# Performance work log

Hardware: AMD Instinct MI355X
Metric: run time of the kernel (lower is better)

## Reference

```python
import jax, jax.numpy as jnp
import numpy as np
import math

V, TB, C, H, L = 50257, 1024, 1024, 16, 8
B, T = 2, 1024
D = C // H


def setup_inputs() -> dict:
    key = jax.random.key(0)
    ks = jax.random.split(key, 16)
    s = 0.02
    n = lambda k, shp: (jax.random.normal(k, shp, jnp.float32) * s)
    inp = {
        "idx": jax.random.randint(ks[0], (B, T), 0, V),
        "tok_emb": n(ks[1], (V, C)),
        "pos_emb": n(ks[2], (1, TB, C)),
        # per-layer stacked params (torch Linear convention: W is [out, in])
        "Wq": n(ks[3], (L, C, C)), "bq": jnp.zeros((L, C)),
        "Wk": n(ks[4], (L, C, C)), "bk": jnp.zeros((L, C)),
        "Wv": n(ks[5], (L, C, C)), "bv": jnp.zeros((L, C)),
        "Wp": n(ks[6], (L, C, C)), "bp": jnp.zeros((L, C)),
        "ln1_w": jnp.ones((L, C)), "ln1_b": jnp.zeros((L, C)),
        "ln2_w": jnp.ones((L, C)), "ln2_b": jnp.zeros((L, C)),
        "W1": n(ks[7], (L, 4 * C, C)), "b1": jnp.zeros((L, 4 * C)),
        "W2": n(ks[8], (L, C, 4 * C)), "b2": jnp.zeros((L, C)),
        "lnf_w": jnp.ones((C,)), "lnf_b": jnp.zeros((C,)),
        "head_w": n(ks[9], (V, C)),
    }
    return inp


def _layer_norm(x, w, b, eps=1e-5):
    mu = x.mean(-1, keepdims=True)
    var = x.var(-1, keepdims=True)
    return (x - mu) * jax.lax.rsqrt(var + eps) * w + b


def _gpt_forward(idx, tok_emb, pos_emb, Wq, bq, Wk, bk, Wv, bv, Wp, bp,
                 ln1_w, ln1_b, ln2_w, ln2_b, W1, b1, W2, b2, lnf_w, lnf_b, head_w):
    b, t = idx.shape
    x = tok_emb[idx] + pos_emb[:, :t, :]  # [B, T, C]; drop = identity (eval)
    causal = jnp.tril(jnp.ones((t, t), dtype=bool))  # [T, T]
    scale = 1.0 / math.sqrt(D)

    def block(x, p):
        (wq, bq_, wk, bk_, wv, bv_, wp, bp_, l1w, l1b, l2w, l2b, w1, b1_, w2, b2_) = p
        h = _layer_norm(x, l1w, l1b)
        q = (h @ wq.T + bq_).reshape(b, t, H, D).transpose(0, 2, 1, 3)  # [B,H,T,D]
        k = (h @ wk.T + bk_).reshape(b, t, H, D).transpose(0, 2, 1, 3)
        v = (h @ wv.T + bv_).reshape(b, t, H, D).transpose(0, 2, 1, 3)
        att = jnp.einsum("bhqd,bhkd->bhqk", q, k) * scale
        att = jnp.where(causal, att, -jnp.inf)
        att = jax.nn.softmax(att, axis=-1)
        y = jnp.einsum("bhqk,bhkd->bhqd", att, v)
        y = y.transpose(0, 2, 1, 3).reshape(b, t, C)
        x = x + (y @ wp.T + bp_)
        h2 = _layer_norm(x, l2w, l2b)
        m = jax.nn.gelu(h2 @ w1.T + b1_, approximate=False)  # torch nn.GELU (erf)
        x = x + (m @ w2.T + b2_)
        return x, None

    params = (Wq, bq, Wk, bk, Wv, bv, Wp, bp, ln1_w, ln1_b, ln2_w, ln2_b, W1, b1, W2, b2)
    x, _ = jax.lax.scan(block, x, params)
    x = _layer_norm(x, lnf_w, lnf_b)
    logits = x @ head_w.T  # [B, T, V]
    return logits


def reference(idx, tok_emb, pos_emb, Wq, bq, Wk, bk, Wv, bv, Wp, bp,
              ln1_w, ln1_b, ln2_w, ln2_b, W1, b1, W2, b2, lnf_w, lnf_b, head_w):
    return _gpt_forward(idx, tok_emb, pos_emb, Wq, bq, Wk, bk, Wv, bv, Wp, bp,
                        ln1_w, ln1_b, ln2_w, ln2_b, W1, b1, W2, b2, lnf_w, lnf_b, head_w)
```

## Files before the change

kernel.cpp:

```cpp
#include <hip/hip_runtime.h>
#include <math.h>

#define V_ 50257
#define C_ 1024
#define H_ 16
#define L_ 8
#define B_ 2
#define T_ 1024
#define BT_ 2048
#define CC_ (C_*C_)
#define QLD_ 3072

typedef unsigned short ushort_t;
using bf16x8 = __attribute__((ext_vector_type(8))) short;
using f32x4  = __attribute__((ext_vector_type(4))) float;

__device__ __forceinline__ ushort_t f2bf(float f){
  union { float f; unsigned u; } a; a.f = f;
  unsigned r = a.u + 0x7fffu + ((a.u >> 16) & 1u);
  return (ushort_t)(r >> 16);
}

__device__ __forceinline__ float wave_sum(float v){
  #pragma unroll
  for(int o=32;o>0;o>>=1) v += __shfl_down(v,o,64);
  return v;
}
__device__ __forceinline__ float wave_max(float v){
  #pragma unroll
  for(int o=32;o>0;o>>=1) v = fmaxf(v, __shfl_down(v,o,64));
  return v;
}

__global__ __launch_bounds__(256) void cvt_blk(const float* __restrict__ s, ushort_t* __restrict__ d,
    long inner4, int nblk, long dstStride4){
  long total = inner4 * nblk;
  for(long i = (long)blockIdx.x*256 + threadIdx.x; i < total; i += (long)gridDim.x*256){
    long blk = i / inner4, r = i - blk*inner4;
    float4 v = ((const float4*)s)[i];
    ushort4 o; o.x=f2bf(v.x); o.y=f2bf(v.y); o.z=f2bf(v.z); o.w=f2bf(v.w);
    ((ushort4*)d)[blk*dstStride4 + r] = o;
  }
}

__global__ __launch_bounds__(256) void pack_qkv_bias(const float* __restrict__ bq,
    const float* __restrict__ bk, const float* __restrict__ bv, float* __restrict__ dst){
  int i = blockIdx.x*256 + threadIdx.x;
  int l = i / QLD_, c = i - l*QLD_;
  float v;
  if(c < C_)            v = bq[l*C_ + c];
  else if(c < 2*C_)     v = bk[l*C_ + c - C_];
  else                  v = bv[l*C_ + c - 2*C_];
  dst[i] = v;
}

__global__ __launch_bounds__(256) void embed_kernel(const int* __restrict__ idx,
    const float* __restrict__ tok, const float* __restrict__ pos, float* __restrict__ x){
  int i = blockIdx.x*256 + threadIdx.x;
  int c = i & (C_-1); int bt = i >> 10; int t = bt & (T_-1);
  x[i] = tok[(size_t)idx[bt]*C_ + c] + pos[t*C_ + c];
}

__global__ __launch_bounds__(256) void ln_kernel(const float* in, const float* __restrict__ w,
    const float* __restrict__ b, float* outF, ushort_t* outB){
  int row = blockIdx.x;
  const float* xr = in + (size_t)row*C_;
  float vals[4]; float sum=0.f, sq=0.f;
  #pragma unroll
  for(int l=0;l<4;l++){ float v = xr[threadIdx.x + l*256]; vals[l]=v; sum+=v; sq+=v*v; }
  __shared__ float r1[4], r2[4];
  float s1 = wave_sum(sum), s2 = wave_sum(sq);
  int wid = threadIdx.x>>6, lane = threadIdx.x&63;
  if(lane==0){ r1[wid]=s1; r2[wid]=s2; }
  __syncthreads();
  float tot  = r1[0]+r1[1]+r1[2]+r1[3];
  float tot2 = r2[0]+r2[1]+r2[2]+r2[3];
  float mu  = tot * (1.f/C_);
  float var = tot2 * (1.f/C_) - mu*mu;
  float inv = rsqrtf(var + 1e-5f);
  #pragma unroll
  for(int l=0;l<4;l++){
    int c = threadIdx.x + l*256;
    float v = (vals[l]-mu)*inv*w[c] + b[c];
    if(outB) outB[(size_t)row*C_ + c] = f2bf(v);
    else     outF[(size_t)row*C_ + c] = v;
  }
}

template<int BN>
__global__ __launch_bounds__(256) void gemm_mfma(
    const ushort_t* __restrict__ A, const ushort_t* __restrict__ W,
    const float* __restrict__ bias, const float* resid,
    float* outF, ushort_t* outB,
    int M, int N, int K, int act)
{
  constexpr int BM = 128;
  constexpr int NSA = BM/16;
  constexpr int NSB = BN/16;
  constexpr int NBF = BN/32;
  __shared__ __align__(16) short sA[2][NSA*512];
  __shared__ __align__(16) short sB[2][NSB*512];
  const int tid  = threadIdx.x;
  const int lane = tid & 63, wid = tid >> 6;
  const int wr = wid >> 1, wc = wid & 1;
  const int m0 = blockIdx.x * BM, n0 = blockIdx.y * BN;
  const int r16 = lane & 15, kq = lane >> 4;

  auto stage = [&](int buf, int k0){
    #pragma unroll
    for(int s2=0; s2<2; ++s2){
      int s = wid*2 + s2;
      const ushort_t* g = A + (size_t)(m0 + s*16 + r16)*K + k0 + kq*8;
      __builtin_amdgcn_global_load_lds((const __attribute__((address_space(1))) void*)g,
          (__attribute__((address_space(3))) void*)&sA[buf][s*512], 16, 0, 0);
    }
    #pragma unroll
    for(int s2=0; s2<NSB/4; ++s2){
      int s = wid*(NSB/4) + s2;
      int gn = n0 + s*16 + r16; if(gn >= N) gn = N-1;
      const ushort_t* g = W + (size_t)gn*K + k0 + kq*8;
      __builtin_amdgcn_global_load_lds((const __attribute__((address_space(1))) void*)g,
          (__attribute__((address_space(3))) void*)&sB[buf][s*512], 16, 0, 0);
    }
  };

  f32x4 acc[4][NBF];
  #pragma unroll
  for(int i=0;i<4;i++)
    #pragma unroll
    for(int j=0;j<NBF;j++) acc[i][j] = (f32x4){0.f,0.f,0.f,0.f};

  const int NT = K >> 5;
  stage(0, 0);
  int cur = 0;
  for(int t=0; t<NT; ++t){
    __syncthreads();
    if(t+1 < NT) stage(cur^1, (t+1)*32);
    bf16x8 af[4], bfr[NBF];
    #pragma unroll
    for(int m=0;m<4;m++) af[m] = *(const bf16x8*)&sA[cur][(wr*4+m)*512 + lane*8];
    #pragma unroll
    for(int n=0;n<NBF;n++) bfr[n] = *(const bf16x8*)&sB[cur][(wc*NBF+n)*512 + lane*8];
    #pragma unroll
    for(int m=0;m<4;m++)
      #pragma unroll
      for(int n=0;n<NBF;n++)
        acc[m][n] = __builtin_amdgcn_mfma_f32_16x16x32_bf16(af[m], bfr[n], acc[m][n], 0, 0, 0);
    cur ^= 1;
  }

  const int colb = n0 + wc*(BN/2);
  #pragma unroll
  for(int m=0;m<4;m++){
    int rowb = m0 + wr*64 + m*16 + kq*4;
    #pragma unroll
    for(int n=0;n<NBF;n++){
      int col = colb + n*16 + r16;
      if(col >= N) continue;
      float bv = bias ? bias[col] : 0.f;
      #pragma unroll
      for(int i=0;i<4;i++){
        int row = rowb + i;
        float v = acc[m][n][i] + bv;
        if(act) v = 0.5f*v*(1.f + erff(v*0.70710678118654752f));
        if(resid) v += resid[(size_t)row*N + col];
        if(outB) outB[(size_t)row*N + col] = f2bf(v);
        else     outF[(size_t)row*N + col] = v;
      }
    }
  }
}

__global__ __launch_bounds__(256) void flash_kernel(const ushort_t* __restrict__ qkv,
    ushort_t* __restrict__ y){
  const int tid = threadIdx.x, lane = tid & 63, wid = tid >> 6;
  const int r16 = lane & 15, kq = lane >> 4;
  const int qt = blockIdx.x, bh = blockIdx.y, b = bh >> 4, h = bh & 15;
  const int q0 = qt*64, qw0 = q0 + wid*16;
  const int qa = qw0 + r16;

  __shared__ __align__(16) short Kt[4][512];
  __shared__ __align__(16) short VT[64][36];
  __shared__ __align__(16) short Pl[4][16][36];
  __shared__ __align__(16) short Ol[4][16][68];

  const size_t rowQ = (size_t)(b*T_ + qw0 + r16)*QLD_ + h*64 + kq*8;
  bf16x8 qf0 = *(const bf16x8*)(qkv + rowQ);
  bf16x8 qf1 = *(const bf16x8*)(qkv + rowQ + 32);

  f32x4 acc[4];
  #pragma unroll
  for(int t=0;t<4;t++) acc[t] = (f32x4){0.f,0.f,0.f,0.f};
  float m_r = -INFINITY, l_r = 0.f;

  const int njt = q0/32 + 2;
  for(int jt=0; jt<njt; ++jt){
    __syncthreads();
    {
      const ushort_t* g = qkv + (size_t)(b*T_ + jt*32 + (wid>>1)*16 + r16)*QLD_
                          + C_ + h*64 + (wid&1)*32 + kq*8;
      __builtin_amdgcn_global_load_lds((const __attribute__((address_space(1))) void*)g,
          (__attribute__((address_space(3))) void*)&Kt[wid][lane*8], 16, 0, 0);
    }
    {
      int k = tid >> 3, d0 = (tid & 7)*8;
      bf16x8 vv = *(const bf16x8*)(qkv + (size_t)(b*T_ + jt*32 + k)*QLD_ + 2*C_ + h*64 + d0);
      #pragma unroll
      for(int j=0;j<8;j++) VT[d0+j][k] = vv[j];
    }
    __syncthreads();

    if(jt*32 <= qw0 + 15){
      f32x4 st0 = (f32x4){0.f,0.f,0.f,0.f}, st1 = st0;
      st0 = __builtin_amdgcn_mfma_f32_16x16x32_bf16(*(const bf16x8*)&Kt[0][lane*8], qf0, st0, 0,0,0);
      st0 = __builtin_amdgcn_mfma_f32_16x16x32_bf16(*(const bf16x8*)&Kt[1][lane*8], qf1, st0, 0,0,0);
      st1 = __builtin_amdgcn_mfma_f32_16x16x32_bf16(*(const bf16x8*)&Kt[2][lane*8], qf0, st1, 0,0,0);
      st1 = __builtin_amdgcn_mfma_f32_16x16x32_bf16(*(const bf16x8*)&Kt[3][lane*8], qf1, st1, 0,0,0);

      float vals[8]; float mx = m_r;
      #pragma unroll
      for(int s=0;s<2;s++){
        #pragma unroll
        for(int i=0;i<4;i++){
          int ka = jt*32 + 16*s + 4*kq + i;
          float v = (s? st1[i] : st0[i]) * 0.125f;
          v = (ka <= qa) ? v : -INFINITY;
          vals[s*4+i] = v; mx = fmaxf(mx, v);
        }
      }
      mx = fmaxf(mx, __shfl_xor(mx, 16, 64));
      mx = fmaxf(mx, __shfl_xor(mx, 32, 64));
      float alpha = __expf(m_r - mx);
      float ps = 0.f;
      #pragma unroll
      for(int idx=0; idx<8; idx++){
        float p = __expf(vals[idx] - mx);
        ps += p;
        Pl[wid][r16][(idx>>2)*16 + 4*kq + (idx&3)] = (short)f2bf(p);
      }
      ps += __shfl_xor(ps, 16, 64);
      ps += __shfl_xor(ps, 32, 64);
      l_r = l_r*alpha + ps; m_r = mx;
      #pragma unroll
      for(int t=0;t<4;t++)
        #pragma unroll
        for(int j=0;j<4;j++) acc[t][j] *= alpha;

      union { bf16x8 v8; uint2 u2[2]; } pf, vf;
      pf.u2[0] = *(const uint2*)&Pl[wid][r16][kq*8];
      pf.u2[1] = *(const uint2*)&Pl[wid][r16][kq*8 + 4];
      #pragma unroll
      for(int db=0; db<4; db++){
        vf.u2[0] = *(const uint2*)&VT[16*db + r16][kq*8];
        vf.u2[1] = *(const uint2*)&VT[16*db + r16][kq*8 + 4];
        acc[db] = __builtin_amdgcn_mfma_f32_16x16x32_bf16(vf.v8, pf.v8, acc[db], 0,0,0);
      }
    }
  }

  float linv = 1.f / l_r;
  #pragma unroll
  for(int db=0; db<4; db++)
    #pragma unroll
    for(int i=0;i<4;i++)
      Ol[wid][r16][16*db + 4*kq + i] = (short)f2bf(acc[db][i]*linv);
  int q = lane >> 2, c0 = (lane & 3)*16;
  const short* src = &Ol[wid][q][c0];
  uint2 a0 = *(const uint2*)(src+0), a1 = *(const uint2*)(src+4);
  uint2 a2 = *(const uint2*)(src+8), a3 = *(const uint2*)(src+12);
  ushort_t* dst = y + (size_t)(b*T_ + qw0 + q)*C_ + h*64 + c0;
  uint4 w0 = {a0.x, a0.y, a1.x, a1.y}, w1 = {a2.x, a2.y, a3.x, a3.y};
  *(uint4*)(dst+0) = w0;
  *(uint4*)(dst+8) = w1;
}

__global__ __launch_bounds__(256) void gemm_nt(const float* __restrict__ A, const float* __restrict__ W,
    const float* __restrict__ bias, const float* resid, float* Cm,
    int M, int N, int K, int act){
  __shared__ float As[16][68];
  __shared__ float Bs[16][68];
  int m0 = blockIdx.y*64, n0 = blockIdx.x*64;
  int tid = threadIdx.x;
  int tx = tid & 15, ty = tid >> 4;
  float acc[4][4] = {};
  for(int k0=0;k0<K;k0+=16){
    #pragma unroll
    for(int l=0;l<4;l++){
      int li = tid + l*256;
      int r = li >> 4, c = li & 15;
      int gm = m0 + r, gn = n0 + r, gk = k0 + c;
      As[c][r] = (gm<M) ? A[(size_t)gm*K + gk] : 0.f;
      Bs[c][r] = (gn<N) ? W[(size_t)gn*K + gk] : 0.f;
    }
    __syncthreads();
    #pragma unroll
    for(int k=0;k<16;k++){
      float4 av = *(const float4*)&As[k][ty*4];
      float4 bv = *(const float4*)&Bs[k][tx*4];
      float a[4] = {av.x, av.y, av.z, av.w};
      float b4[4] = {bv.x, bv.y, bv.z, bv.w};
      #pragma unroll
      for(int i=0;i<4;i++)
        #pragma unroll
        for(int j=0;j<4;j++)
          acc[i][j] = fmaf(a[i], b4[j], acc[i][j]);
    }
    __syncthreads();
  }
  #pragma unroll
  for(int i=0;i<4;i++){
    int m = m0 + ty*4 + i; if(m>=M) continue;
    #pragma unroll
    for(int j=0;j<4;j++){
      int n = n0 + tx*4 + j; if(n>=N) continue;
      float v = acc[i][j];
      if(bias) v += bias[n];
      if(act)  v = 0.5f*v*(1.f + erff(v*0.70710678118654752f));
      if(resid) v += resid[(size_t)m*N + n];
      Cm[(size_t)m*N + n] = v;
    }
  }
}

extern "C" void kernel_launch(void* const* d_in, const int* in_sizes, int n_in,
                              void* d_out, int out_size, void* d_ws, size_t ws_size,
                              hipStream_t stream) {
  const int*   idx  = (const int*)  d_in[0];
  const float* tok  = (const float*)d_in[1];
  const float* pos  = (const float*)d_in[2];
  const float* Wq   = (const float*)d_in[3];
  const float* bq   = (const float*)d_in[4];
  const float* Wk   = (const float*)d_in[5];
  const float* bk   = (const float*)d_in[6];
  const float* Wv   = (const float*)d_in[7];
  const float* bv   = (const float*)d_in[8];
  const float* Wp   = (const float*)d_in[9];
  const float* bp   = (const float*)d_in[10];
  const float* ln1w = (const float*)d_in[11];
  const float* ln1b = (const float*)d_in[12];
  const float* ln2w = (const float*)d_in[13];
  const float* ln2b = (const float*)d_in[14];
  const float* W1   = (const float*)d_in[15];
  const float* b1   = (const float*)d_in[16];
  const float* W2   = (const float*)d_in[17];
  const float* b2   = (const float*)d_in[18];
  const float* lnfw = (const float*)d_in[19];
  const float* lnfb = (const float*)d_in[20];
  const float* headw= (const float*)d_in[21];

  float* out = (float*)d_out;
  ushort_t* qkvb = (ushort_t*)(out);
  ushort_t* hb   = (ushort_t*)(out + 3145728);
  ushort_t* yb   = (ushort_t*)(out + 4194304);
  ushort_t* mb   = (ushort_t*)(out + 5242880);
  ushort_t* wqkv = (ushort_t*)(out + 9437184);
  ushort_t* wpb  = (ushort_t*)(out + 22020096);
  ushort_t* w1b  = (ushort_t*)(out + 26214400);
  ushort_t* w2b  = (ushort_t*)(out + 42991616);
  float*    bqkv = out + 59768832;
  float*    x    = (float*)d_ws;
  ushort_t* xb   = (ushort_t*)((float*)d_ws + 2097152);
  ushort_t* whb  = (ushort_t*)((float*)d_ws + 3145728);
  const bool big = ws_size >= (size_t)28877312 * 4;

  cvt_blk<<<2048,256,0,stream>>>(Wq, wqkv,          CC_/4, L_, 3*CC_/4);
  cvt_blk<<<2048,256,0,stream>>>(Wk, wqkv + CC_,    CC_/4, L_, 3*CC_/4);
  cvt_blk<<<2048,256,0,stream>>>(Wv, wqkv + 2*CC_,  CC_/4, L_, 3*CC_/4);
  cvt_blk<<<2048,256,0,stream>>>(Wp, wpb,  (long)L_*CC_/4,   1, (long)L_*CC_/4);
  cvt_blk<<<2048,256,0,stream>>>(W1, w1b,  (long)L_*CC_,     1, (long)L_*CC_);
  cvt_blk<<<2048,256,0,stream>>>(W2, w2b,  (long)L_*CC_,     1, (long)L_*CC_);
  if(big) cvt_blk<<<2048,256,0,stream>>>(headw, whb, (long)V_*C_/4, 1, (long)V_*C_/4);
  pack_qkv_bias<<<L_*QLD_/256,256,0,stream>>>(bq, bk, bv, bqkv);

  embed_kernel<<<BT_*C_/256, 256, 0, stream>>>(idx, tok, pos, x);

  for(int l=0;l<L_;l++){
    ln_kernel<<<BT_,256,0,stream>>>(x, ln1w + l*C_, ln1b + l*C_, nullptr, hb);
    gemm_mfma<128><<<dim3(BT_/128, QLD_/128),256,0,stream>>>(hb, wqkv + (size_t)l*3*CC_,
        bqkv + l*QLD_, nullptr, nullptr, qkvb, BT_, QLD_, C_, 0);
    flash_kernel<<<dim3(T_/64, B_*H_),256,0,stream>>>(qkvb, yb);
    gemm_mfma<64><<<dim3(BT_/128, C_/64),256,0,stream>>>(yb, wpb + (size_t)l*CC_,
        bp + l*C_, x, x, nullptr, BT_, C_, C_, 0);
    ln_kernel<<<BT_,256,0,stream>>>(x, ln2w + l*C_, ln2b + l*C_, nullptr, hb);
    gemm_mfma<128><<<dim3(BT_/128, 4*C_/128),256,0,stream>>>(hb, w1b + (size_t)l*4*CC_,
        b1 + (size_t)l*4*C_, nullptr, nullptr, mb, BT_, 4*C_, C_, 1);
    gemm_mfma<64><<<dim3(BT_/128, C_/64),256,0,stream>>>(mb, w2b + (size_t)l*4*CC_,
        b2 + l*C_, x, x, nullptr, BT_, C_, 4*C_, 0);
  }

  if(big){
    ln_kernel<<<BT_,256,0,stream>>>(x, lnfw, lnfb, nullptr, xb);
    gemm_mfma<128><<<dim3(BT_/128, (V_+127)/128),256,0,stream>>>(xb, whb,
        nullptr, nullptr, out, nullptr, BT_, V_, C_, 0);
  } else {
    ln_kernel<<<BT_,256,0,stream>>>(x, lnfw, lnfb, x, nullptr);
    gemm_nt<<<dim3((V_+63)/64, BT_/64),256,0,stream>>>(x, headw, nullptr, nullptr, out,
                                                       BT_, V_, C_, 0);
  }
}
```

Before: 2.921 ms.

## Widen flash-attention key tiles, add MFMA priority hints, enlarge LM-head tile

The flash kernel now processes 64 keys per iteration instead of 32. Causal masking is applied only on the diagonal tile, and P is written to LDS with packed stores. s_setprio brackets are placed around the MFMA sections in both the GEMM and attention kernels. The LM-head GEMM switches to BN=256 tiles and writes logits with nontemporal stores. Together these aim to cut loop and sync overhead and reduce cache pollution from the large output, at the cost of more LDS and registers per block, which may lower occupancy.

```diff
diff --git a/kernel.cpp b/kernel.cpp
--- a/kernel.cpp
+++ b/kernel.cpp
@@ -24,11 +24,6 @@
 __device__ __forceinline__ float wave_sum(float v){
   #pragma unroll
   for(int o=32;o>0;o>>=1) v += __shfl_down(v,o,64);
-  return v;
-}
-__device__ __forceinline__ float wave_max(float v){
-  #pragma unroll
-  for(int o=32;o>0;o>>=1) v = fmaxf(v, __shfl_down(v,o,64));
   return v;
 }
 
@@ -92,13 +87,12 @@
     const ushort_t* __restrict__ A, const ushort_t* __restrict__ W,
     const float* __restrict__ bias, const float* resid,
     float* outF, ushort_t* outB,
-    int M, int N, int K, int act)
+    int M, int N, int K, int act, int nt)
 {
   constexpr int BM = 128;
-  constexpr int NSA = BM/16;
   constexpr int NSB = BN/16;
   constexpr int NBF = BN/32;
-  __shared__ __align__(16) short sA[2][NSA*512];
+  __shared__ __align__(16) short sA[2][8*512];
   __shared__ __align__(16) short sB[2][NSB*512];
   const int tid  = threadIdx.x;
   const int lane = tid & 63, wid = tid >> 6;
@@ -141,11 +135,13 @@
     for(int m=0;m<4;m++) af[m] = *(const bf16x8*)&sA[cur][(wr*4+m)*512 + lane*8];
     #pragma unroll
     for(int n=0;n<NBF;n++) bfr[n] = *(const bf16x8*)&sB[cur][(wc*NBF+n)*512 + lane*8];
+    __builtin_amdgcn_s_setprio(1);
     #pragma unroll
     for(int m=0;m<4;m++)
       #pragma unroll
       for(int n=0;n<NBF;n++)
         acc[m][n] = __builtin_amdgcn_mfma_f32_16x16x32_bf16(af[m], bfr[n], acc[m][n], 0, 0, 0);
+    __builtin_amdgcn_s_setprio(0);
     cur ^= 1;
   }
 
@@ -165,7 +161,8 @@
         if(act) v = 0.5f*v*(1.f + erff(v*0.70710678118654752f));
         if(resid) v += resid[(size_t)row*N + col];
         if(outB) outB[(size_t)row*N + col] = f2bf(v);
-        else     outF[(size_t)row*N + col] = v;
+        else if(nt) __builtin_nontemporal_store(v, &outF[(size_t)row*N + col]);
+        else outF[(size_t)row*N + col] = v;
       }
     }
   }
@@ -179,12 +176,12 @@
   const int q0 = qt*64, qw0 = q0 + wid*16;
   const int qa = qw0 + r16;
 
-  __shared__ __align__(16) short Kt[4][512];
-  __shared__ __align__(16) short VT[64][36];
-  __shared__ __align__(16) short Pl[4][16][36];
+  __shared__ __align__(16) short Kt[8][512];
+  __shared__ __align__(16) short VT[64][68];
+  __shared__ __align__(16) short Pl[4][16][68];
   __shared__ __align__(16) short Ol[4][16][68];
 
-  const size_t rowQ = (size_t)(b*T_ + qw0 + r16)*QLD_ + h*64 + kq*8;
+  const size_t rowQ = (size_t)(b*T_ + qa)*QLD_ + h*64 + kq*8;
   bf16x8 qf0 = *(const bf16x8*)(qkv + rowQ);
   bf16x8 qf1 = *(const bf16x8*)(qkv + rowQ + 32);
 
@@ -193,69 +190,91 @@
   for(int t=0;t<4;t++) acc[t] = (f32x4){0.f,0.f,0.f,0.f};
   float m_r = -INFINITY, l_r = 0.f;
 
-  const int njt = q0/32 + 2;
+  const int njt = qt + 1;
   for(int jt=0; jt<njt; ++jt){
     __syncthreads();
-    {
-      const ushort_t* g = qkv + (size_t)(b*T_ + jt*32 + (wid>>1)*16 + r16)*QLD_
-                          + C_ + h*64 + (wid&1)*32 + kq*8;
+    #pragma unroll
+    for(int s2=0;s2<2;s2++){
+      int s = wid*2 + s2;
+      const ushort_t* g = qkv + (size_t)(b*T_ + jt*64 + (s>>1)*16 + r16)*QLD_
+                          + C_ + h*64 + (s&1)*32 + kq*8;
       __builtin_amdgcn_global_load_lds((const __attribute__((address_space(1))) void*)g,
-          (__attribute__((address_space(3))) void*)&Kt[wid][lane*8], 16, 0, 0);
-    }
-    {
-      int k = tid >> 3, d0 = (tid & 7)*8;
-      bf16x8 vv = *(const bf16x8*)(qkv + (size_t)(b*T_ + jt*32 + k)*QLD_ + 2*C_ + h*64 + d0);
-      #pragma unroll
-      for(int j=0;j<8;j++) VT[d0+j][k] = vv[j];
+          (__attribute__((address_space(3))) void*)&Kt[s][lane*8], 16, 0, 0);
+    }
+    #pragma unroll
+    for(int a2=0;a2<2;a2++){
+      int d0 = (a2*4 + wid)*8;
+      bf16x8 vv = *(const bf16x8*)(qkv + (size_t)(b*T_ + jt*64 + lane)*QLD_ + 2*C_ + h*64 + d0);
+      #pragma unroll
+      for(int j=0;j<8;j++) VT[d0+j][lane] = vv[j];
     }
     __syncthreads();
 
-    if(jt*32 <= qw0 + 15){
-      f32x4 st0 = (f32x4){0.f,0.f,0.f,0.f}, st1 = st0;
-      st0 = __builtin_amdgcn_mfma_f32_16x16x32_bf16(*(const bf16x8*)&Kt[0][lane*8], qf0, st0, 0,0,0);
-      st0 = __builtin_amdgcn_mfma_f32_16x16x32_bf16(*(const bf16x8*)&Kt[1][lane*8], qf1, st0, 0,0,0);
-      st1 = __builtin_amdgcn_mfma_f32_16x16x32_bf16(*(const bf16x8*)&Kt[2][lane*8], qf0, st1, 0,0,0);
-      st1 = __builtin_amdgcn_mfma_f32_16x16x32_bf16(*(const bf16x8*)&Kt[3][lane*8], qf1, st1, 0,0,0);
-
-      float vals[8]; float mx = m_r;
-      #pragma unroll
-      for(int s=0;s<2;s++){
+    f32x4 st[4];
+    __builtin_amdgcn_s_setprio(1);
+    #pragma unroll
+    for(int kr=0;kr<4;kr++){
+      st[kr] = (f32x4){0.f,0.f,0.f,0.f};
+      st[kr] = __builtin_amdgcn_mfma_f32_16x16x32_bf16(*(const bf16x8*)&Kt[kr*2+0][lane*8], qf0, st[kr], 0,0,0);
+      st[kr] = __builtin_amdgcn_mfma_f32_16x16x32_bf16(*(const bf16x8*)&Kt[kr*2+1][lane*8], qf1, st[kr], 0,0,0);
+    }
+    __builtin_amdgcn_s_setprio(0);
+
+    float vals[16]; float mx = m_r;
+    if(jt == njt-1){
+      #pragma unroll
+      for(int kr=0;kr<4;kr++)
         #pragma unroll
         for(int i=0;i<4;i++){
-          int ka = jt*32 + 16*s + 4*kq + i;
-          float v = (s? st1[i] : st0[i]) * 0.125f;
-          v = (ka <= qa) ? v : -INFINITY;
-          vals[s*4+i] = v; mx = fmaxf(mx, v);
+          int ka = jt*64 + kr*16 + 4*kq + i;
+          float v = (ka <= qa) ? st[kr][i]*0.125f : -INFINITY;
+          vals[kr*4+i] = v; mx = fmaxf(mx, v);
         }
-      }
-      mx = fmaxf(mx, __shfl_xor(mx, 16, 64));
-      mx = fmaxf(mx, __shfl_xor(mx, 32, 64));
-      float alpha = __expf(m_r - mx);
-      float ps = 0.f;
-      #pragma unroll
-      for(int idx=0; idx<8; idx++){
-        float p = __expf(vals[idx] - mx);
-        ps += p;
-        Pl[wid][r16][(idx>>2)*16 + 4*kq + (idx&3)] = (short)f2bf(p);
-      }
-      ps += __shfl_xor(ps, 16, 64);
-      ps += __shfl_xor(ps, 32, 64);
-      l_r = l_r*alpha + ps; m_r = mx;
-      #pragma unroll
-      for(int t=0;t<4;t++)
+    } else {
+      #pragma unroll
+      for(int kr=0;kr<4;kr++)
         #pragma unroll
-        for(int j=0;j<4;j++) acc[t][j] *= alpha;
-
-      union { bf16x8 v8; uint2 u2[2]; } pf, vf;
-      pf.u2[0] = *(const uint2*)&Pl[wid][r16][kq*8];
-      pf.u2[1] = *(const uint2*)&Pl[wid][r16][kq*8 + 4];
+        for(int i=0;i<4;i++){
+          float v = st[kr][i]*0.125f;
+          vals[kr*4+i] = v; mx = fmaxf(mx, v);
+        }
+    }
+    mx = fmaxf(mx, __shfl_xor(mx, 16, 64));
+    mx = fmaxf(mx, __shfl_xor(mx, 32, 64));
+    float alpha = __expf(m_r - mx);
+    float ps = 0.f;
+    #pragma unroll
+    for(int kr=0;kr<4;kr++){
+      float p0 = __expf(vals[kr*4+0]-mx), p1 = __expf(vals[kr*4+1]-mx);
+      float p2 = __expf(vals[kr*4+2]-mx), p3 = __expf(vals[kr*4+3]-mx);
+      ps += (p0+p1)+(p2+p3);
+      unsigned u0 = (unsigned)f2bf(p0) | ((unsigned)f2bf(p1)<<16);
+      unsigned u1 = (unsigned)f2bf(p2) | ((unsigned)f2bf(p3)<<16);
+      *(unsigned*)&Pl[wid][r16][kr*16 + 4*kq]     = u0;
+      *(unsigned*)&Pl[wid][r16][kr*16 + 4*kq + 2] = u1;
+    }
+    ps += __shfl_xor(ps, 16, 64);
+    ps += __shfl_xor(ps, 32, 64);
+    l_r = l_r*alpha + ps; m_r = mx;
+    #pragma unroll
+    for(int t=0;t<4;t++)
+      #pragma unroll
+      for(int j=0;j<4;j++) acc[t][j] *= alpha;
+
+    union { bf16x8 v8; uint2 u2[2]; } pf, vf;
+    __builtin_amdgcn_s_setprio(1);
+    #pragma unroll
+    for(int ks2=0; ks2<2; ks2++){
+      pf.u2[0] = *(const uint2*)&Pl[wid][r16][ks2*32 + kq*8];
+      pf.u2[1] = *(const uint2*)&Pl[wid][r16][ks2*32 + kq*8 + 4];
       #pragma unroll
       for(int db=0; db<4; db++){
-        vf.u2[0] = *(const uint2*)&VT[16*db + r16][kq*8];
-        vf.u2[1] = *(const uint2*)&VT[16*db + r16][kq*8 + 4];
+        vf.u2[0] = *(const uint2*)&VT[16*db + r16][ks2*32 + kq*8];
+        vf.u2[1] = *(const uint2*)&VT[16*db + r16][ks2*32 + kq*8 + 4];
         acc[db] = __builtin_amdgcn_mfma_f32_16x16x32_bf16(vf.v8, pf.v8, acc[db], 0,0,0);
       }
     }
+    __builtin_amdgcn_s_setprio(0);
   }
 
   float linv = 1.f / l_r;
@@ -377,21 +396,21 @@
   for(int l=0;l<L_;l++){
     ln_kernel<<<BT_,256,0,stream>>>(x, ln1w + l*C_, ln1b + l*C_, nullptr, hb);
     gemm_mfma<128><<<dim3(BT_/128, QLD_/128),256,0,stream>>>(hb, wqkv + (size_t)l*3*CC_,
-        bqkv + l*QLD_, nullptr, nullptr, qkvb, BT_, QLD_, C_, 0);
+        bqkv + l*QLD_, nullptr, nullptr, qkvb, BT_, QLD_, C_, 0, 0);
     flash_kernel<<<dim3(T_/64, B_*H_),256,0,stream>>>(qkvb, yb);
     gemm_mfma<64><<<dim3(BT_/128, C_/64),256,0,stream>>>(yb, wpb + (size_t)l*CC_,
-        bp + l*C_, x, x, nullptr, BT_, C_, C_, 0);
+        bp + l*C_, x, x, nullptr, BT_, C_, C_, 0, 0);
     ln_kernel<<<BT_,256,0,stream>>>(x, ln2w + l*C_, ln2b + l*C_, nullptr, hb);
     gemm_mfma<128><<<dim3(BT_/128, 4*C_/128),256,0,stream>>>(hb, w1b + (size_t)l*4*CC_,
-        b1 + (size_t)l*4*C_, nullptr, nullptr, mb, BT_, 4*C_, C_, 1);
+        b1 + (size_t)l*4*C_, nullptr, nullptr, mb, BT_, 4*C_, C_, 1, 0);
     gemm_mfma<64><<<dim3(BT_/128, C_/64),256,0,stream>>>(mb, w2b + (size_t)l*4*CC_,
-        b2 + l*C_, x, x, nullptr, BT_, C_, 4*C_, 0);
+        b2 + l*C_, x, x, nullptr, BT_, C_, 4*C_, 0, 0);
   }
 
   if(big){
     ln_kernel<<<BT_,256,0,stream>>>(x, lnfw, lnfb, nullptr, xb);
-    gemm_mfma<128><<<dim3(BT_/128, (V_+127)/128),256,0,stream>>>(xb, whb,
-        nullptr, nullptr, out, nullptr, BT_, V_, C_, 0);
+    gemm_mfma<256><<<dim3(BT_/128, (V_+255)/256),256,0,stream>>>(xb, whb,
+        nullptr, nullptr, out, nullptr, BT_, V_, C_, 0, 1);
   } else {
     ln_kernel<<<BT_,256,0,stream>>>(x, lnfw, lnfb, x, nullptr);
     gemm_nt<<<dim3((V_+63)/64, BT_/64),256,0,stream>>>(x, headw, nullptr, nullptr, out,
```

Measured after the change: 3.081 ms. 5.5% more time.
